# Optimization experiments

Hardware: AMD Instinct MI355X
Metric: run time of the kernel (lower is better)

The kernel has to match this reference:

```python
import jax, jax.numpy as jnp
import numpy as np

H = 2048      # hidden_size
NH = 16       # num attention heads
KVH = 4       # num kv heads (GQA)
D = 128       # head_dim
E = 32        # num experts
K = 4         # top-k experts per token
I = 768       # moe intermediate size
T = 1024      # num tokens (single prefill sequence)
EPS = 1e-6
THETA = 10000.0


def rmsnorm(x, w, eps=EPS):
    return x * jax.lax.rsqrt(jnp.mean(x * x, axis=-1, keepdims=True) + eps) * w


def rope_cos_sin(positions, dim, theta):
    inv_freq = 1.0 / (theta ** (jnp.arange(0, dim, 2, dtype=jnp.float32) / dim))
    freqs = positions.astype(jnp.float32)[:, None] * inv_freq[None, :]   # [T, D/2]
    emb = jnp.concatenate([freqs, freqs], axis=-1)                       # [T, D]
    return jnp.cos(emb), jnp.sin(emb)


def apply_rope(x, cos, sin):
    # x: [T, nH, D]; cos/sin: [T, D] -> neox style: cat(-x2, x1)
    x1, x2 = jnp.split(x, 2, axis=-1)
    x_rot = jnp.concatenate([-x2, x1], axis=-1)
    return cos[:, None, :] * x + sin[:, None, :] * x_rot


def setup_inputs() -> dict:
    key = jax.random.key(0)
    ks = jax.random.split(key, 8)
    s = 0.02
    return {
        "hidden_states": jax.random.normal(ks[0], (T, H), jnp.float32),
        "positions": jnp.arange(T, dtype=jnp.int32),
        "ln1_w": jnp.ones((H,), jnp.float32),
        "w_qkv": jax.random.normal(ks[1], ((NH + 2 * KVH) * D, H), jnp.float32) * s,
        "q_norm_w": jnp.ones((D,), jnp.float32),
        "k_norm_w": jnp.ones((D,), jnp.float32),
        "w_o": jax.random.normal(ks[2], (H, NH * D), jnp.float32) * s,
        "ln2_w": jnp.ones((H,), jnp.float32),
        "router_w": jax.random.normal(ks[3], (E, H), jnp.float32) * s,
        "w_gate": jax.random.normal(ks[4], (E, I, H), jnp.float32) * s,
        "w_up": jax.random.normal(ks[5], (E, I, H), jnp.float32) * s,
        "w_down": jax.random.normal(ks[6], (E, H, I), jnp.float32) * s,
    }


def decoder_layer(hidden_states, positions, ln1_w, w_qkv, q_norm_w, k_norm_w,
                  w_o, ln2_w, router_w, w_gate, w_up, w_down):
    # ---- attention block ----
    residual = hidden_states
    h = rmsnorm(hidden_states, ln1_w)

    qkv = h @ w_qkv.T                                      # [T, (NH+2*KVH)*D]
    q, k, v = jnp.split(qkv, [NH * D, (NH + KVH) * D], axis=-1)
    q = q.reshape(T, NH, D)
    k = k.reshape(T, KVH, D)
    v = v.reshape(T, KVH, D)

    # per-head RMSNorm on q and k (Qwen3 QK-norm)
    q = rmsnorm(q, q_norm_w)
    k = rmsnorm(k, k_norm_w)

    cos, sin = rope_cos_sin(positions, D, THETA)
    q = apply_rope(q, cos, sin)
    k = apply_rope(k, cos, sin)

    rep = NH // KVH
    k = jnp.repeat(k, rep, axis=1)                         # [T, NH, D]
    v = jnp.repeat(v, rep, axis=1)

    scale = D ** -0.5
    scores = jnp.einsum("qhd,khd->hqk", q, k) * scale      # [NH, T, T]
    causal = jnp.tril(jnp.ones((T, T), bool))
    scores = jnp.where(causal[None], scores, -1e30)
    probs = jax.nn.softmax(scores, axis=-1)
    attn = jnp.einsum("hqk,khd->qhd", probs, v).reshape(T, NH * D)
    attn_out = attn @ w_o.T                                # [T, H]

    hidden = residual + attn_out

    # ---- MoE block ----
    residual = hidden
    h = rmsnorm(hidden, ln2_w)

    logits = h @ router_w.T                                # [T, E]
    router_probs = jax.nn.softmax(logits, axis=-1)
    topk_w, topk_idx = jax.lax.top_k(router_probs, K)      # softmax-then-topk
    topk_w = topk_w / (jnp.sum(topk_w, axis=-1, keepdims=True) + 1e-20)

    # scatter top-k weights into a dense [T, E] combine matrix
    combine = jnp.zeros((T, E), h.dtype).at[
        jnp.arange(T)[:, None], topk_idx].add(topk_w)

    gate = jnp.einsum("th,eih->tei", h, w_gate)            # [T, E, I]
    up = jnp.einsum("th,eih->tei", h, w_up)
    act = jax.nn.silu(gate) * up
    moe_out = jnp.einsum("tei,ehi,te->th", act, w_down, combine)

    return residual + moe_out


def reference(hidden_states, positions, ln1_w, w_qkv, q_norm_w, k_norm_w,
              w_o, ln2_w, router_w, w_gate, w_up, w_down):
    return decoder_layer(hidden_states, positions, ln1_w, w_qkv, q_norm_w,
                         k_norm_w, w_o, ln2_w, router_w, w_gate, w_up, w_down)
```

## Files before the change

kernel.cpp:

```cpp
#include <hip/hip_runtime.h>

typedef __attribute__((ext_vector_type(4))) float f32x4;
typedef __attribute__((ext_vector_type(8))) __bf16 bf16x8;
typedef __attribute__((ext_vector_type(4))) __bf16 bf16x4;

__device__ __forceinline__ f32x4 mfma16(bf16x8 a, bf16x8 b, f32x4 c) {
  return __builtin_amdgcn_mfma_f32_16x16x32_bf16(a, b, c, 0, 0, 0);
}

__global__ __launch_bounds__(256) void rmsnorm_k(const float* __restrict__ x,
                                                 const float* __restrict__ w,
                                                 float* __restrict__ y,
                                                 __bf16* __restrict__ yb) {
  int t = blockIdx.x;
  const float* xr = x + (size_t)t * 2048;
  int d0 = threadIdx.x * 4;
  float4 v1 = *(const float4*)(xr + d0);
  float4 v2 = *(const float4*)(xr + 1024 + d0);
  float ss = v1.x*v1.x + v1.y*v1.y + v1.z*v1.z + v1.w*v1.w
           + v2.x*v2.x + v2.y*v2.y + v2.z*v2.z + v2.w*v2.w;
#pragma unroll
  for (int mk = 1; mk < 64; mk <<= 1) ss += __shfl_xor(ss, mk);
  __shared__ float red[4];
  if ((threadIdx.x & 63) == 0) red[threadIdx.x >> 6] = ss;
  __syncthreads();
  float tot = red[0] + red[1] + red[2] + red[3];
  float rs = rsqrtf(tot * (1.0f / 2048.0f) + 1e-6f);
  float* yr = y + (size_t)t * 2048;
  float4 w1 = *(const float4*)(w + d0);
  float4 w2 = *(const float4*)(w + 1024 + d0);
  float4 o1, o2;
  o1.x = v1.x*rs*w1.x; o1.y = v1.y*rs*w1.y; o1.z = v1.z*rs*w1.z; o1.w = v1.w*rs*w1.w;
  o2.x = v2.x*rs*w2.x; o2.y = v2.y*rs*w2.y; o2.z = v2.z*rs*w2.z; o2.w = v2.w*rs*w2.w;
  *(float4*)(yr + d0) = o1;
  *(float4*)(yr + 1024 + d0) = o2;
  if (yb) {
    bf16x4 b1, b2;
    b1[0] = (__bf16)o1.x; b1[1] = (__bf16)o1.y; b1[2] = (__bf16)o1.z; b1[3] = (__bf16)o1.w;
    b2[0] = (__bf16)o2.x; b2[1] = (__bf16)o2.y; b2[2] = (__bf16)o2.z; b2[3] = (__bf16)o2.w;
    *(bf16x4*)(yb + (size_t)t * 2048 + d0) = b1;
    *(bf16x4*)(yb + (size_t)t * 2048 + 1024 + d0) = b2;
  }
}

__global__ __launch_bounds__(256) void gemm3_k(const float* __restrict__ A,
                                               const float* __restrict__ B,
                                               const float* __restrict__ RESID,
                                               float* __restrict__ C, int N, int K) {
  __shared__ __align__(16) __bf16 sm[4 * 128 * 40];
  const int m0 = blockIdx.x * 128, n0 = blockIdx.y * 128;
  const int tid = threadIdx.x, l = tid & 63, w = tid >> 6;
  const int wm = w >> 1, wn = w & 1;
  __bf16* Ah = sm;         __bf16* Al = sm + 5120;
  __bf16* Bh = sm + 10240; __bf16* Bl = sm + 15360;
  f32x4 acc[4][4] = {};
  for (int kt = 0; kt < K; kt += 32) {
    __syncthreads();
#pragma unroll
    for (int i = 0; i < 4; i++) {
      int c = tid + i * 256;
      int row = c >> 3, k4 = c & 7;
      float4 v = *(const float4*)(A + (size_t)(m0 + row) * K + kt + k4 * 4);
      bf16x4 hv, lv;
#pragma unroll
      for (int j = 0; j < 4; j++) {
        float f = ((const float*)&v)[j];
        __bf16 h = (__bf16)f; hv[j] = h; lv[j] = (__bf16)(f - (float)h);
      }
      *(bf16x4*)(Ah + row * 40 + k4 * 4) = hv;
      *(bf16x4*)(Al + row * 40 + k4 * 4) = lv;
      float4 u = *(const float4*)(B + (size_t)(n0 + row) * K + kt + k4 * 4);
      bf16x4 hu, lu;
#pragma unroll
      for (int j = 0; j < 4; j++) {
        float f = ((const float*)&u)[j];
        __bf16 h = (__bf16)f; hu[j] = h; lu[j] = (__bf16)(f - (float)h);
      }
      *(bf16x4*)(Bh + row * 40 + k4 * 4) = hu;
      *(bf16x4*)(Bl + row * 40 + k4 * 4) = lu;
    }
    __syncthreads();
    bf16x8 ah[4], al[4], bh[4], bl[4];
    const int ko = (l >> 4) * 8;
#pragma unroll
    for (int f = 0; f < 4; f++) {
      int ar = wm * 64 + f * 16 + (l & 15);
      int br = wn * 64 + f * 16 + (l & 15);
      ah[f] = *(const bf16x8*)(Ah + ar * 40 + ko);
      al[f] = *(const bf16x8*)(Al + ar * 40 + ko);
      bh[f] = *(const bf16x8*)(Bh + br * 40 + ko);
      bl[f] = *(const bf16x8*)(Bl + br * 40 + ko);
    }
#pragma unroll
    for (int mf = 0; mf < 4; mf++)
#pragma unroll
      for (int nf = 0; nf < 4; nf++) {
        acc[mf][nf] = mfma16(ah[mf], bh[nf], acc[mf][nf]);
        acc[mf][nf] = mfma16(ah[mf], bl[nf], acc[mf][nf]);
        acc[mf][nf] = mfma16(al[mf], bh[nf], acc[mf][nf]);
      }
  }
#pragma unroll
  for (int mf = 0; mf < 4; mf++) {
    int row = m0 + wm * 64 + mf * 16 + ((l >> 4) << 2);
#pragma unroll
    for (int nf = 0; nf < 4; nf++) {
      int col = n0 + wn * 64 + nf * 16 + (l & 15);
#pragma unroll
      for (int r = 0; r < 4; r++) {
        float v = acc[mf][nf][r];
        if (RESID) v += RESID[(size_t)(row + r) * N + col];
        C[(size_t)(row + r) * N + col] = v;
      }
    }
  }
}

__global__ __launch_bounds__(128) void qkr_k(const float* __restrict__ qkv,
                                             const int* __restrict__ pos,
                                             const float* __restrict__ qw,
                                             const float* __restrict__ kw,
                                             __bf16* __restrict__ qh, __bf16* __restrict__ ql,
                                             __bf16* __restrict__ kh, __bf16* __restrict__ kl,
                                             __bf16* __restrict__ vh, __bf16* __restrict__ vl) {
  int hs = blockIdx.x, t = blockIdx.y, d = threadIdx.x;
  float x = qkv[(size_t)t * 3072 + hs * 128 + d];
  __shared__ float xs[128];
  __shared__ float red[2];
  float o;
  if (hs < 20) {
    float ss = x * x;
#pragma unroll
    for (int mk = 1; mk < 64; mk <<= 1) ss += __shfl_xor(ss, mk);
    if ((d & 63) == 0) red[d >> 6] = ss;
    __syncthreads();
    float rs = rsqrtf((red[0] + red[1]) * (1.0f / 128.0f) + 1e-6f);
    const float* w = (hs < 16) ? qw : kw;
    float xn = x * rs * w[d];
    xs[d] = xn;
    __syncthreads();
    int i = d & 63;
    float invf = (float)pow(10000.0, -(double)i / 64.0);
    float ang = (float)pos[t] * invf;
    float cf = (float)cos((double)ang);
    float sf = (float)sin((double)ang);
    float rot = (d < 64) ? -xs[d + 64] : xs[d - 64];
    o = cf * xn + sf * rot;
  } else {
    o = x;
  }
  __bf16 hi = (__bf16)o;
  __bf16 lo = (__bf16)(o - (float)hi);
  if (hs < 16) {
    size_t idx = ((size_t)hs * 1024 + t) * 128 + d;
    qh[idx] = hi; ql[idx] = lo;
  } else if (hs < 20) {
    size_t idx = ((size_t)(hs - 16) * 1024 + t) * 128 + d;
    kh[idx] = hi; kl[idx] = lo;
  } else {
    size_t idx = ((size_t)(hs - 20) * 1024 + t) * 128 + d;
    vh[idx] = hi; vl[idx] = lo;
  }
}

__global__ void vtrans_k(const __bf16* __restrict__ vh, const __bf16* __restrict__ vl,
                         __bf16* __restrict__ vhT, __bf16* __restrict__ vlT) {
  __shared__ __bf16 tile[32][33];
  int kv = blockIdx.z, t0 = blockIdx.x * 32, d0 = blockIdx.y * 32;
  int tx = threadIdx.x, ty = threadIdx.y;
  tile[ty][tx] = vh[((size_t)kv * 1024 + t0 + ty) * 128 + d0 + tx];
  __syncthreads();
  vhT[((size_t)kv * 128 + d0 + ty) * 1024 + t0 + tx] = tile[tx][ty];
  __syncthreads();
  tile[ty][tx] = vl[((size_t)kv * 1024 + t0 + ty) * 128 + d0 + tx];
  __syncthreads();
  vlT[((size_t)kv * 128 + d0 + ty) * 1024 + t0 + tx] = tile[tx][ty];
}

__global__ __launch_bounds__(256) void flash_k(const __bf16* __restrict__ qh, const __bf16* __restrict__ ql,
                                               const __bf16* __restrict__ kh, const __bf16* __restrict__ kl,
                                               const __bf16* __restrict__ vhT, const __bf16* __restrict__ vlT,
                                               float* __restrict__ attn) {
  constexpr int KH = 0, KL = 4352, VH = 8704, VL = 13824, PH = 18944, PL = 21504;
  __shared__ __align__(16) __bf16 sm[24064];
  const int qt = blockIdx.x, h = blockIdx.y;
  const int q0 = qt * 64, kvh = h >> 2;
  const int tid = threadIdx.x, l = tid & 63, w = tid >> 6;
  for (int c = tid; c < 1024; c += 256) {
    int row = c >> 4, dc = c & 15;
    size_t g = ((size_t)h * 1024 + q0 + row) * 128 + dc * 8;
// ... 130 lines not shown
    float mx = v;
#pragma unroll
    for (int mk = 1; mk < 32; mk <<= 1) mx = fmaxf(mx, __shfl_xor(mx, mk));
    float ex = (l < 32) ? expf(v - mx) : 0.0f;
    float den = ex;
#pragma unroll
    for (int mk = 1; mk < 32; mk <<= 1) den += __shfl_xor(den, mk);
    float prob = ex / den;
    float pv = v;
    int sel_i[4]; float sel_w[4]; float wsum = 0.0f;
#pragma unroll
    for (int j = 0; j < 4; j++) {
      float m2 = pv;
#pragma unroll
      for (int mk = 1; mk < 32; mk <<= 1) m2 = fmaxf(m2, __shfl_xor(m2, mk));
      unsigned long long ball = __ballot((pv == m2) && (l < 32));
      int sel = __ffsll(ball) - 1;
      float ps = __shfl(prob, sel);
      sel_i[j] = sel; sel_w[j] = ps; wsum += ps;
      if (l == sel) pv = -3e38f;
    }
    if (l < 4) {
      tidx[t * 4 + l] = sel_i[l];
      tw[t * 4 + l] = sel_w[l] / (wsum + 1e-20f);
      atomicAdd(&counts[sel_i[l]], 1);
    }
  }
}

__global__ void zero_k(int* counts) { if (threadIdx.x < 32) counts[threadIdx.x] = 0; }

__global__ void scan_k(const int* __restrict__ counts, int* __restrict__ offs,
                       int* __restrict__ cursor, int* __restrict__ pair_e,
                       int* __restrict__ pair_mt) {
  int l = threadIdx.x;
  int c = (l < 32) ? counts[l] : 0;
  int x = c;
#pragma unroll
  for (int d = 1; d < 32; d <<= 1) {
    int y = __shfl_up(x, d);
    if (l >= d) x += y;
  }
  if (l < 32) { offs[l] = x - c; cursor[l] = 0; }
  if (l == 31) offs[32] = x;
  if (l == 0) {
    int n = 0;
    for (int e = 0; e < 32; e++) {
      int ce = counts[e];
      for (int m = 0; m * 128 < ce; m++) { pair_e[n] = e; pair_mt[n] = m; n++; }
    }
    for (; n < 64; n++) { pair_e[n] = -1; pair_mt[n] = 0; }
  }
}

__global__ __launch_bounds__(256) void scatter_k(const int* __restrict__ tidx,
                                                 const int* __restrict__ offs,
                                                 int* __restrict__ cursor,
                                                 int* __restrict__ row_of_slot,
                                                 int* __restrict__ tok_of_row) {
  int p = blockIdx.x * 256 + threadIdx.x;
  if (p >= 4096) return;
  int e = tidx[p];
  int pos = atomicAdd(&cursor[e], 1);
  int row = offs[e] + pos;
  row_of_slot[p] = row;
  tok_of_row[row] = p >> 2;
}

__global__ __launch_bounds__(256) void gateup_k(const __bf16* __restrict__ h2b,
                                                const float* __restrict__ wg,
                                                const float* __restrict__ wu,
                                                const int* __restrict__ counts,
                                                const int* __restrict__ offs,
                                                const int* __restrict__ tok_of_row,
                                                const int* __restrict__ pair_e,
                                                const int* __restrict__ pair_mt,
                                                float* __restrict__ gu) {
  const int p = blockIdx.y;
  const int e = pair_e[p];
  if (e < 0) return;
  const int mt = pair_mt[p];
  const int cnt = counts[e];
  const int j = blockIdx.x;
  const float* wsel = (j < 6) ? wg : wu;
  const int n0 = (j < 6 ? j : j - 6) * 128;
  const int gout = (j < 6) ? 0 : 768;
  __shared__ __align__(16) __bf16 smA[128 * 40];
  __shared__ __align__(16) __bf16 smB[128 * 40];
  __shared__ int toks[128];
  const int tid = threadIdx.x, l = tid & 63, w = tid >> 6;
  const int wm = w >> 1, wn = w & 1;
  if (tid < 128) {
    int r = mt * 128 + tid;
    toks[tid] = (r < cnt) ? tok_of_row[offs[e] + r] : tok_of_row[offs[e]];
  }
  __syncthreads();
  const float* we = wsel + (size_t)e * 768 * 2048;
  bf16x8 ra[2]; float4 rb[4];
#pragma unroll
  for (int i = 0; i < 2; i++) {
    int c = tid + i * 256, row = c >> 2, kc = c & 3;
    ra[i] = *(const bf16x8*)(h2b + (size_t)toks[row] * 2048 + kc * 8);
  }
#pragma unroll
  for (int i = 0; i < 4; i++) {
    int c = tid + i * 256, row = c >> 3, k4 = c & 7;
    rb[i] = *(const float4*)(we + (size_t)(n0 + row) * 2048 + k4 * 4);
  }
  f32x4 acc[4][4] = {};
  for (int kt = 0; kt < 2048; kt += 32) {
    __syncthreads();
#pragma unroll
    for (int i = 0; i < 2; i++) {
      int c = tid + i * 256, row = c >> 2, kc = c & 3;
      *(bf16x8*)(smA + row * 40 + kc * 8) = ra[i];
    }
#pragma unroll
    for (int i = 0; i < 4; i++) {
      int c = tid + i * 256, row = c >> 3, k4 = c & 7;
      bf16x4 hv;
#pragma unroll
      for (int q = 0; q < 4; q++) hv[q] = (__bf16)((const float*)&rb[i])[q];
      *(bf16x4*)(smB + row * 40 + k4 * 4) = hv;
    }
    __syncthreads();
    if (kt + 32 < 2048) {
#pragma unroll
      for (int i = 0; i < 2; i++) {
        int c = tid + i * 256, row = c >> 2, kc = c & 3;
        ra[i] = *(const bf16x8*)(h2b + (size_t)toks[row] * 2048 + kt + 32 + kc * 8);
      }
#pragma unroll
      for (int i = 0; i < 4; i++) {
        int c = tid + i * 256, row = c >> 3, k4 = c & 7;
        rb[i] = *(const float4*)(we + (size_t)(n0 + row) * 2048 + kt + 32 + k4 * 4);
      }
    }
    bf16x8 af[4], bf_[4];
    const int ko = (l >> 4) * 8;
#pragma unroll
    for (int f = 0; f < 4; f++) {
      af[f]  = *(const bf16x8*)(smA + (wm * 64 + f * 16 + (l & 15)) * 40 + ko);
      bf_[f] = *(const bf16x8*)(smB + (wn * 64 + f * 16 + (l & 15)) * 40 + ko);
    }
#pragma unroll
    for (int mf = 0; mf < 4; mf++)
#pragma unroll
      for (int nf = 0; nf < 4; nf++)
        acc[mf][nf] = mfma16(af[mf], bf_[nf], acc[mf][nf]);
  }
#pragma unroll
  for (int mf = 0; mf < 4; mf++) {
    int rr = mt * 128 + wm * 64 + mf * 16 + ((l >> 4) << 2);
#pragma unroll
    for (int nf = 0; nf < 4; nf++) {
      int col = gout + n0 + wn * 64 + nf * 16 + (l & 15);
#pragma unroll
      for (int r = 0; r < 4; r++)
        if (rr + r < cnt)
          gu[(size_t)(offs[e] + rr + r) * 1536 + col] = acc[mf][nf][r];
    }
  }
}

__global__ __launch_bounds__(192) void silu_k(const float* __restrict__ gu,
                                              __bf16* __restrict__ act) {
  int r = blockIdx.x, c = threadIdx.x * 4;
  float4 g = *(const float4*)(gu + (size_t)r * 1536 + c);
  float4 u = *(const float4*)(gu + (size_t)r * 1536 + 768 + c);
  bf16x4 o;
  o[0] = (__bf16)(g.x / (1.0f + expf(-g.x)) * u.x);
  o[1] = (__bf16)(g.y / (1.0f + expf(-g.y)) * u.y);
  o[2] = (__bf16)(g.z / (1.0f + expf(-g.z)) * u.z);
  o[3] = (__bf16)(g.w / (1.0f + expf(-g.w)) * u.w);
  *(bf16x4*)(act + (size_t)r * 768 + c) = o;
}

__global__ __launch_bounds__(256) void down_k(const __bf16* __restrict__ act,
                                              const float* __restrict__ wd,
                                              const int* __restrict__ counts,
                                              const int* __restrict__ offs,
                                              const int* __restrict__ pair_e,
                                              const int* __restrict__ pair_mt,
                                              float* __restrict__ dout) {
  const int p = blockIdx.y;
  const int e = pair_e[p];
  if (e < 0) return;
  const int mt = pair_mt[p];
  const int cnt = counts[e];
  const int n0 = blockIdx.x * 128;
  __shared__ __align__(16) __bf16 smA[128 * 40];
  __shared__ __align__(16) __bf16 smB[128 * 40];
  const int tid = threadIdx.x, l = tid & 63, w = tid >> 6;
  const int wm = w >> 1, wn = w & 1;
  const float* wde = wd + (size_t)e * 2048 * 768;
  const int base = offs[e] + mt * 128;
  bf16x8 ra[2]; float4 rb[4];
#pragma unroll
  for (int i = 0; i < 2; i++) {
    int c = tid + i * 256, row = c >> 2, kc = c & 3;
    int rg = base + row; if (rg > 4095) rg = 4095;
    ra[i] = *(const bf16x8*)(act + (size_t)rg * 768 + kc * 8);
  }
#pragma unroll
  for (int i = 0; i < 4; i++) {
    int c = tid + i * 256, row = c >> 3, k4 = c & 7;
    rb[i] = *(const float4*)(wde + (size_t)(n0 + row) * 768 + k4 * 4);
  }
  f32x4 acc[4][4] = {};
  for (int kt = 0; kt < 768; kt += 32) {
    __syncthreads();
#pragma unroll
    for (int i = 0; i < 2; i++) {
      int c = tid + i * 256, row = c >> 2, kc = c & 3;
      *(bf16x8*)(smA + row * 40 + kc * 8) = ra[i];
    }
#pragma unroll
    for (int i = 0; i < 4; i++) {
      int c = tid + i * 256, row = c >> 3, k4 = c & 7;
      bf16x4 hv;
#pragma unroll
      for (int q = 0; q < 4; q++) hv[q] = (__bf16)((const float*)&rb[i])[q];
      *(bf16x4*)(smB + row * 40 + k4 * 4) = hv;
    }
    __syncthreads();
    if (kt + 32 < 768) {
#pragma unroll
      for (int i = 0; i < 2; i++) {
        int c = tid + i * 256, row = c >> 2, kc = c & 3;
        int rg = base + row; if (rg > 4095) rg = 4095;
        ra[i] = *(const bf16x8*)(act + (size_t)rg * 768 + kt + 32 + kc * 8);
      }
#pragma unroll
      for (int i = 0; i < 4; i++) {
        int c = tid + i * 256, row = c >> 3, k4 = c & 7;
        rb[i] = *(const float4*)(wde + (size_t)(n0 + row) * 768 + kt + 32 + k4 * 4);
      }
    }
    bf16x8 af[4], bf_[4];
    const int ko = (l >> 4) * 8;
#pragma unroll
    for (int f = 0; f < 4; f++) {
      af[f]  = *(const bf16x8*)(smA + (wm * 64 + f * 16 + (l & 15)) * 40 + ko);
      bf_[f] = *(const bf16x8*)(smB + (wn * 64 + f * 16 + (l & 15)) * 40 + ko);
    }
#pragma unroll
    for (int mf = 0; mf < 4; mf++)
#pragma unroll
      for (int nf = 0; nf < 4; nf++)
        acc[mf][nf] = mfma16(af[mf], bf_[nf], acc[mf][nf]);
  }
#pragma unroll
  for (int mf = 0; mf < 4; mf++) {
    int rr = mt * 128 + wm * 64 + mf * 16 + ((l >> 4) << 2);
#pragma unroll
    for (int nf = 0; nf < 4; nf++) {
      int col = n0 + wn * 64 + nf * 16 + (l & 15);
#pragma unroll
      for (int r = 0; r < 4; r++)
        if (rr + r < cnt)
          dout[(size_t)(offs[e] + rr + r) * 2048 + col] = acc[mf][nf][r];
    }
  }
}

__global__ __launch_bounds__(256) void combine_k(const float* __restrict__ hidden,
                                                 const float* __restrict__ dout,
                                                 const int* __restrict__ row_of_slot,
                                                 const float* __restrict__ tw,
                                                 float* __restrict__ out) {
  int t = blockIdx.x;
  int r0 = row_of_slot[t * 4 + 0], r1 = row_of_slot[t * 4 + 1];
  int r2 = row_of_slot[t * 4 + 2], r3 = row_of_slot[t * 4 + 3];
  float w0 = tw[t * 4 + 0], w1 = tw[t * 4 + 1], w2 = tw[t * 4 + 2], w3 = tw[t * 4 + 3];
  const float* h = hidden + (size_t)t * 2048;
  float* o = out + (size_t)t * 2048;
  for (int d = threadIdx.x * 4; d < 2048; d += 1024) {
    float4 hv = *(const float4*)(h + d);
    float4 a0 = *(const float4*)(dout + (size_t)r0 * 2048 + d);
    float4 a1 = *(const float4*)(dout + (size_t)r1 * 2048 + d);
    float4 a2 = *(const float4*)(dout + (size_t)r2 * 2048 + d);
    float4 a3 = *(const float4*)(dout + (size_t)r3 * 2048 + d);
    float4 ov;
    ov.x = hv.x + w0 * a0.x + w1 * a1.x + w2 * a2.x + w3 * a3.x;
    ov.y = hv.y + w0 * a0.y + w1 * a1.y + w2 * a2.y + w3 * a3.y;
    ov.z = hv.z + w0 * a0.z + w1 * a1.z + w2 * a2.z + w3 * a3.z;
    ov.w = hv.w + w0 * a0.w + w1 * a1.w + w2 * a2.w + w3 * a3.w;
    *(float4*)(o + d) = ov;
  }
}

extern "C" void kernel_launch(void* const* d_in, const int* in_sizes, int n_in,
                              void* d_out, int out_size, void* d_ws, size_t ws_size,
                              hipStream_t stream) {
  (void)in_sizes; (void)n_in; (void)out_size; (void)ws_size;
  const float* hs   = (const float*)d_in[0];
  const int*   pos  = (const int*)d_in[1];
  const float* ln1w = (const float*)d_in[2];
  const float* wqkv = (const float*)d_in[3];
  const float* qnw  = (const float*)d_in[4];
  const float* knw  = (const float*)d_in[5];
  const float* wo   = (const float*)d_in[6];
  const float* ln2w = (const float*)d_in[7];
  const float* rw   = (const float*)d_in[8];
  const float* wg   = (const float*)d_in[9];
  const float* wu   = (const float*)d_in[10];
  const float* wd   = (const float*)d_in[11];
  float* out = (float*)d_out;
  char* ws = (char*)d_ws;

  float*  h1     = (float*)(ws + 0);
  float*  gu     = (float*)(ws + 0);
  float*  dout   = (float*)(ws + 0);
  float*  qkv    = (float*)(ws + 8388608);
  __bf16* qh     = (__bf16*)(ws + 20971520);
  __bf16* ql     = (__bf16*)(ws + 25165824);
  __bf16* kh     = (__bf16*)(ws + 29360128);
  __bf16* kl     = (__bf16*)(ws + 30408704);
  __bf16* vh     = (__bf16*)(ws + 31457280);
  __bf16* vl     = (__bf16*)(ws + 32505856);
  __bf16* vhT    = (__bf16*)(ws + 33554432);
  __bf16* vlT    = (__bf16*)(ws + 34603008);
  int*    pair_e = (int*)(ws + 33554432);
  int*    pair_mt= (int*)(ws + 33554944);
  float*  attn   = (float*)(ws + 35651584);
  __bf16* h2b    = (__bf16*)(ws + 35651584);
  __bf16* act    = (__bf16*)(ws + 35651584);
  float*  hidden = (float*)(ws + 44040192);
  float*  h2     = (float*)(ws + 52428800);
  int*    tidx   = (int*)(ws + 60817408);
  float*  tw     = (float*)(ws + 60833792);
  int*    counts = (int*)(ws + 60850176);
  int*    offs   = (int*)(ws + 60850432);
  int*    cursor = (int*)(ws + 60850688);
  int*    row_of_slot = (int*)(ws + 60850944);
  int*    tok_of_row  = (int*)(ws + 60867328);

  rmsnorm_k<<<1024, 256, 0, stream>>>(hs, ln1w, h1, nullptr);
  gemm3_k<<<dim3(8, 24), 256, 0, stream>>>(h1, wqkv, nullptr, qkv, 3072, 2048);
  qkr_k<<<dim3(24, 1024), 128, 0, stream>>>(qkv, pos, qnw, knw, qh, ql, kh, kl, vh, vl);
  vtrans_k<<<dim3(32, 4, 4), dim3(32, 32), 0, stream>>>(vh, vl, vhT, vlT);
  flash_k<<<dim3(16, 16), 256, 0, stream>>>(qh, ql, kh, kl, vhT, vlT, attn);
  gemm3_k<<<dim3(8, 16), 256, 0, stream>>>(attn, wo, hs, hidden, 2048, 2048);

  rmsnorm_k<<<1024, 256, 0, stream>>>(hidden, ln2w, h2, h2b);
  zero_k<<<1, 64, 0, stream>>>(counts);
  router_k<<<1024, 256, 0, stream>>>(h2, rw, tidx, tw, counts);
  scan_k<<<1, 64, 0, stream>>>(counts, offs, cursor, pair_e, pair_mt);
  scatter_k<<<16, 256, 0, stream>>>(tidx, offs, cursor, row_of_slot, tok_of_row);
  gateup_k<<<dim3(12, 64), 256, 0, stream>>>(h2b, wg, wu, counts, offs, tok_of_row, pair_e, pair_mt, gu);
  silu_k<<<4096, 192, 0, stream>>>(gu, act);
  down_k<<<dim3(16, 64), 256, 0, stream>>>(act, wd, counts, offs, pair_e, pair_mt, dout);
  combine_k<<<1024, 256, 0, stream>>>(hidden, dout, row_of_slot, tw, out);
}
```

Measured before the change: 658.0 us.

## Halve GEMM N-tile to 64 and add register prefetch to dense GEMM

Shrinks the N tile of the dense split-bf16 GEMM and the MoE gate/up and down GEMMs from 128 to 64 columns, doubling grid size so more workgroups fill the CUs. The dense GEMM also gains a register double-buffer that loads the next K-slice from global memory while the current slice is being computed. Smaller tiles mean the A tile is reloaded twice as often, which adds global traffic and lowers arithmetic intensity per block.

```diff
diff --git a/kernel.cpp b/kernel.cpp
--- a/kernel.cpp
+++ b/kernel.cpp
@@ -47,54 +47,82 @@
                                                const float* __restrict__ B,
                                                const float* __restrict__ RESID,
                                                float* __restrict__ C, int N, int K) {
-  __shared__ __align__(16) __bf16 sm[4 * 128 * 40];
-  const int m0 = blockIdx.x * 128, n0 = blockIdx.y * 128;
+  __shared__ __align__(16) __bf16 smAh[128 * 40];
+  __shared__ __align__(16) __bf16 smAl[128 * 40];
+  __shared__ __align__(16) __bf16 smBh[64 * 40];
+  __shared__ __align__(16) __bf16 smBl[64 * 40];
+  const int m0 = blockIdx.x * 128, n0 = blockIdx.y * 64;
   const int tid = threadIdx.x, l = tid & 63, w = tid >> 6;
   const int wm = w >> 1, wn = w & 1;
-  __bf16* Ah = sm;         __bf16* Al = sm + 5120;
-  __bf16* Bh = sm + 10240; __bf16* Bl = sm + 15360;
-  f32x4 acc[4][4] = {};
+  float4 ra[4], rb[2];
+#pragma unroll
+  for (int i = 0; i < 4; i++) {
+    int c = tid + i * 256, row = c >> 3, k4 = c & 7;
+    ra[i] = *(const float4*)(A + (size_t)(m0 + row) * K + k4 * 4);
+  }
+#pragma unroll
+  for (int i = 0; i < 2; i++) {
+    int c = tid + i * 256, row = c >> 3, k4 = c & 7;
+    rb[i] = *(const float4*)(B + (size_t)(n0 + row) * K + k4 * 4);
+  }
+  f32x4 acc[4][2] = {};
   for (int kt = 0; kt < K; kt += 32) {
     __syncthreads();
 #pragma unroll
     for (int i = 0; i < 4; i++) {
-      int c = tid + i * 256;
-      int row = c >> 3, k4 = c & 7;
-      float4 v = *(const float4*)(A + (size_t)(m0 + row) * K + kt + k4 * 4);
+      int c = tid + i * 256, row = c >> 3, k4 = c & 7;
       bf16x4 hv, lv;
 #pragma unroll
       for (int j = 0; j < 4; j++) {
-        float f = ((const float*)&v)[j];
+        float f = ((const float*)&ra[i])[j];
         __bf16 h = (__bf16)f; hv[j] = h; lv[j] = (__bf16)(f - (float)h);
       }
-      *(bf16x4*)(Ah + row * 40 + k4 * 4) = hv;
-      *(bf16x4*)(Al + row * 40 + k4 * 4) = lv;
-      float4 u = *(const float4*)(B + (size_t)(n0 + row) * K + kt + k4 * 4);
-      bf16x4 hu, lu;
+      *(bf16x4*)(smAh + row * 40 + k4 * 4) = hv;
+      *(bf16x4*)(smAl + row * 40 + k4 * 4) = lv;
+    }
+#pragma unroll
+    for (int i = 0; i < 2; i++) {
+      int c = tid + i * 256, row = c >> 3, k4 = c & 7;
+      bf16x4 hv, lv;
 #pragma unroll
       for (int j = 0; j < 4; j++) {
-        float f = ((const float*)&u)[j];
-        __bf16 h = (__bf16)f; hu[j] = h; lu[j] = (__bf16)(f - (float)h);
-      }
-      *(bf16x4*)(Bh + row * 40 + k4 * 4) = hu;
-      *(bf16x4*)(Bl + row * 40 + k4 * 4) = lu;
-    }
-    __syncthreads();
-    bf16x8 ah[4], al[4], bh[4], bl[4];
+        float f = ((const float*)&rb[i])[j];
+        __bf16 h = (__bf16)f; hv[j] = h; lv[j] = (__bf16)(f - (float)h);
+      }
+      *(bf16x4*)(smBh + row * 40 + k4 * 4) = hv;
+      *(bf16x4*)(smBl + row * 40 + k4 * 4) = lv;
+    }
+    __syncthreads();
+    if (kt + 32 < K) {
+#pragma unroll
+      for (int i = 0; i < 4; i++) {
+        int c = tid + i * 256, row = c >> 3, k4 = c & 7;
+        ra[i] = *(const float4*)(A + (size_t)(m0 + row) * K + kt + 32 + k4 * 4);
+      }
+#pragma unroll
+      for (int i = 0; i < 2; i++) {
+        int c = tid + i * 256, row = c >> 3, k4 = c & 7;
+        rb[i] = *(const float4*)(B + (size_t)(n0 + row) * K + kt + 32 + k4 * 4);
+      }
+    }
+    bf16x8 ah[4], al[4], bh[2], bl[2];
     const int ko = (l >> 4) * 8;
 #pragma unroll
     for (int f = 0; f < 4; f++) {
       int ar = wm * 64 + f * 16 + (l & 15);
-      int br = wn * 64 + f * 16 + (l & 15);
-      ah[f] = *(const bf16x8*)(Ah + ar * 40 + ko);
-      al[f] = *(const bf16x8*)(Al + ar * 40 + ko);
-      bh[f] = *(const bf16x8*)(Bh + br * 40 + ko);
-      bl[f] = *(const bf16x8*)(Bl + br * 40 + ko);
+      ah[f] = *(const bf16x8*)(smAh + ar * 40 + ko);
+      al[f] = *(const bf16x8*)(smAl + ar * 40 + ko);
+    }
+#pragma unroll
+    for (int f = 0; f < 2; f++) {
+      int br = wn * 32 + f * 16 + (l & 15);
+      bh[f] = *(const bf16x8*)(smBh + br * 40 + ko);
+      bl[f] = *(const bf16x8*)(smBl + br * 40 + ko);
     }
 #pragma unroll
     for (int mf = 0; mf < 4; mf++)
 #pragma unroll
-      for (int nf = 0; nf < 4; nf++) {
+      for (int nf = 0; nf < 2; nf++) {
         acc[mf][nf] = mfma16(ah[mf], bh[nf], acc[mf][nf]);
         acc[mf][nf] = mfma16(ah[mf], bl[nf], acc[mf][nf]);
         acc[mf][nf] = mfma16(al[mf], bh[nf], acc[mf][nf]);
@@ -104,8 +132,8 @@
   for (int mf = 0; mf < 4; mf++) {
     int row = m0 + wm * 64 + mf * 16 + ((l >> 4) << 2);
 #pragma unroll
-    for (int nf = 0; nf < 4; nf++) {
-      int col = n0 + wn * 64 + nf * 16 + (l & 15);
+    for (int nf = 0; nf < 2; nf++) {
+      int col = n0 + wn * 32 + nf * 16 + (l & 15);
 #pragma unroll
       for (int r = 0; r < 4; r++) {
         float v = acc[mf][nf][r];
@@ -402,11 +430,11 @@
   const int mt = pair_mt[p];
   const int cnt = counts[e];
   const int j = blockIdx.x;
-  const float* wsel = (j < 6) ? wg : wu;
-  const int n0 = (j < 6 ? j : j - 6) * 128;
-  const int gout = (j < 6) ? 0 : 768;
+  const float* wsel = (j < 12) ? wg : wu;
+  const int n0 = (j < 12 ? j : j - 12) * 64;
+  const int gout = (j < 12) ? 0 : 768;
   __shared__ __align__(16) __bf16 smA[128 * 40];
-  __shared__ __align__(16) __bf16 smB[128 * 40];
+  __shared__ __align__(16) __bf16 smB[64 * 40];
   __shared__ int toks[128];
   const int tid = threadIdx.x, l = tid & 63, w = tid >> 6;
   const int wm = w >> 1, wn = w & 1;
@@ -416,18 +444,18 @@
   }
   __syncthreads();
   const float* we = wsel + (size_t)e * 768 * 2048;
-  bf16x8 ra[2]; float4 rb[4];
+  bf16x8 ra[2]; float4 rb[2];
 #pragma unroll
   for (int i = 0; i < 2; i++) {
     int c = tid + i * 256, row = c >> 2, kc = c & 3;
     ra[i] = *(const bf16x8*)(h2b + (size_t)toks[row] * 2048 + kc * 8);
   }
 #pragma unroll
-  for (int i = 0; i < 4; i++) {
+  for (int i = 0; i < 2; i++) {
     int c = tid + i * 256, row = c >> 3, k4 = c & 7;
     rb[i] = *(const float4*)(we + (size_t)(n0 + row) * 2048 + k4 * 4);
   }
-  f32x4 acc[4][4] = {};
+  f32x4 acc[4][2] = {};
   for (int kt = 0; kt < 2048; kt += 32) {
     __syncthreads();
 #pragma unroll
@@ -436,7 +464,7 @@
       *(bf16x8*)(smA + row * 40 + kc * 8) = ra[i];
     }
 #pragma unroll
-    for (int i = 0; i < 4; i++) {
+    for (int i = 0; i < 2; i++) {
       int c = tid + i * 256, row = c >> 3, k4 = c & 7;
       bf16x4 hv;
 #pragma unroll
@@ -451,30 +479,31 @@
         ra[i] = *(const bf16x8*)(h2b + (size_t)toks[row] * 2048 + kt + 32 + kc * 8);
       }
 #pragma unroll
-      for (int i = 0; i < 4; i++) {
+      for (int i = 0; i < 2; i++) {
         int c = tid + i * 256, row = c >> 3, k4 = c & 7;
         rb[i] = *(const float4*)(we + (size_t)(n0 + row) * 2048 + kt + 32 + k4 * 4);
       }
     }
-    bf16x8 af[4], bf_[4];
+    bf16x8 af[4], bf_[2];
     const int ko = (l >> 4) * 8;
 #pragma unroll
-    for (int f = 0; f < 4; f++) {
-      af[f]  = *(const bf16x8*)(smA + (wm * 64 + f * 16 + (l & 15)) * 40 + ko);
-      bf_[f] = *(const bf16x8*)(smB + (wn * 64 + f * 16 + (l & 15)) * 40 + ko);
-    }
+    for (int f = 0; f < 4; f++)
+      af[f] = *(const bf16x8*)(smA + (wm * 64 + f * 16 + (l & 15)) * 40 + ko);
+#pragma unroll
+    for (int f = 0; f < 2; f++)
+      bf_[f] = *(const bf16x8*)(smB + (wn * 32 + f * 16 + (l & 15)) * 40 + ko);
 #pragma unroll
     for (int mf = 0; mf < 4; mf++)
 #pragma unroll
-      for (int nf = 0; nf < 4; nf++)
+      for (int nf = 0; nf < 2; nf++)
         acc[mf][nf] = mfma16(af[mf], bf_[nf], acc[mf][nf]);
   }
 #pragma unroll
   for (int mf = 0; mf < 4; mf++) {
     int rr = mt * 128 + wm * 64 + mf * 16 + ((l >> 4) << 2);
 #pragma unroll
-    for (int nf = 0; nf < 4; nf++) {
-      int col = gout + n0 + wn * 64 + nf * 16 + (l & 15);
+    for (int nf = 0; nf < 2; nf++) {
+      int col = gout + n0 + wn * 32 + nf * 16 + (l & 15);
 #pragma unroll
       for (int r = 0; r < 4; r++)
         if (rr + r < cnt)
@@ -508,14 +537,14 @@
   if (e < 0) return;
   const int mt = pair_mt[p];
   const int cnt = counts[e];
-  const int n0 = blockIdx.x * 128;
+  const int n0 = blockIdx.x * 64;
   __shared__ __align__(16) __bf16 smA[128 * 40];
-  __shared__ __align__(16) __bf16 smB[128 * 40];
+  __shared__ __align__(16) __bf16 smB[64 * 40];
   const int tid = threadIdx.x, l = tid & 63, w = tid >> 6;
   const int wm = w >> 1, wn = w & 1;
   const float* wde = wd + (size_t)e * 2048 * 768;
   const int base = offs[e] + mt * 128;
-  bf16x8 ra[2]; float4 rb[4];
+  bf16x8 ra[2]; float4 rb[2];
 #pragma unroll
   for (int i = 0; i < 2; i++) {
     int c = tid + i * 256, row = c >> 2, kc = c & 3;
@@ -523,11 +552,11 @@
     ra[i] = *(const bf16x8*)(act + (size_t)rg * 768 + kc * 8);
   }
 #pragma unroll
-  for (int i = 0; i < 4; i++) {
+  for (int i = 0; i < 2; i++) {
     int c = tid + i * 256, row = c >> 3, k4 = c & 7;
     rb[i] = *(const float4*)(wde + (size_t)(n0 + row) * 768 + k4 * 4);
   }
-  f32x4 acc[4][4] = {};
+  f32x4 acc[4][2] = {};
   for (int kt = 0; kt < 768; kt += 32) {
     __syncthreads();
 #pragma unroll
@@ -536,7 +565,7 @@
       *(bf16x8*)(smA + row * 40 + kc * 8) = ra[i];
     }
 #pragma unroll
-    for (int i = 0; i < 4; i++) {
+    for (int i = 0; i < 2; i++) {
       int c = tid + i * 256, row = c >> 3, k4 = c & 7;
       bf16x4 hv;
 #pragma unroll
@@ -552,30 +581,31 @@
         ra[i] = *(const bf16x8*)(act + (size_t)rg * 768 + kt + 32 + kc * 8);
       }
 #pragma unroll
-      for (int i = 0; i < 4; i++) {
+      for (int i = 0; i < 2; i++) {
         int c = tid + i * 256, row = c >> 3, k4 = c & 7;
         rb[i] = *(const float4*)(wde + (size_t)(n0 + row) * 768 + kt + 32 + k4 * 4);
       }
     }
-    bf16x8 af[4], bf_[4];
+    bf16x8 af[4], bf_[2];
     const int ko = (l >> 4) * 8;
 #pragma unroll
-    for (int f = 0; f < 4; f++) {
-      af[f]  = *(const bf16x8*)(smA + (wm * 64 + f * 16 + (l & 15)) * 40 + ko);
-      bf_[f] = *(const bf16x8*)(smB + (wn * 64 + f * 16 + (l & 15)) * 40 + ko);
-    }
+    for (int f = 0; f < 4; f++)
+      af[f] = *(const bf16x8*)(smA + (wm * 64 + f * 16 + (l & 15)) * 40 + ko);
+#pragma unroll
+    for (int f = 0; f < 2; f++)
+      bf_[f] = *(const bf16x8*)(smB + (wn * 32 + f * 16 + (l & 15)) * 40 + ko);
 #pragma unroll
     for (int mf = 0; mf < 4; mf++)
 #pragma unroll
-      for (int nf = 0; nf < 4; nf++)
+      for (int nf = 0; nf < 2; nf++)
         acc[mf][nf] = mfma16(af[mf], bf_[nf], acc[mf][nf]);
   }
 #pragma unroll
   for (int mf = 0; mf < 4; mf++) {
     int rr = mt * 128 + wm * 64 + mf * 16 + ((l >> 4) << 2);
 #pragma unroll
-    for (int nf = 0; nf < 4; nf++) {
-      int col = n0 + wn * 64 + nf * 16 + (l & 15);
+    for (int nf = 0; nf < 2; nf++) {
+      int col = n0 + wn * 32 + nf * 16 + (l & 15);
 #pragma unroll
       for (int r = 0; r < 4; r++)
         if (rr + r < cnt)
@@ -657,19 +687,19 @@
   int*    tok_of_row  = (int*)(ws + 60867328);
 
   rmsnorm_k<<<1024, 256, 0, stream>>>(hs, ln1w, h1, nullptr);
-  gemm3_k<<<dim3(8, 24), 256, 0, stream>>>(h1, wqkv, nullptr, qkv, 3072, 2048);
+  gemm3_k<<<dim3(8, 48), 256, 0, stream>>>(h1, wqkv, nullptr, qkv, 3072, 2048);
   qkr_k<<<dim3(24, 1024), 128, 0, stream>>>(qkv, pos, qnw, knw, qh, ql, kh, kl, vh, vl);
   vtrans_k<<<dim3(32, 4, 4), dim3(32, 32), 0, stream>>>(vh, vl, vhT, vlT);
   flash_k<<<dim3(16, 16), 256, 0, stream>>>(qh, ql, kh, kl, vhT, vlT, attn);
-  gemm3_k<<<dim3(8, 16), 256, 0, stream>>>(attn, wo, hs, hidden, 2048, 2048);
+  gemm3_k<<<dim3(8, 32), 256, 0, stream>>>(attn, wo, hs, hidden, 2048, 2048);
 
   rmsnorm_k<<<1024, 256, 0, stream>>>(hidden, ln2w, h2, h2b);
   zero_k<<<1, 64, 0, stream>>>(counts);
   router_k<<<1024, 256, 0, stream>>>(h2, rw, tidx, tw, counts);
   scan_k<<<1, 64, 0, stream>>>(counts, offs, cursor, pair_e, pair_mt);
   scatter_k<<<16, 256, 0, stream>>>(tidx, offs, cursor, row_of_slot, tok_of_row);
-  gateup_k<<<dim3(12, 64), 256, 0, stream>>>(h2b, wg, wu, counts, offs, tok_of_row, pair_e, pair_mt, gu);
+  gateup_k<<<dim3(24, 64), 256, 0, stream>>>(h2b, wg, wu, counts, offs, tok_of_row, pair_e, pair_mt, gu);
   silu_k<<<4096, 192, 0, stream>>>(gu, act);
-  down_k<<<dim3(16, 64), 256, 0, stream>>>(act, wd, counts, offs, pair_e, pair_mt, dout);
+  down_k<<<dim3(32, 64), 256, 0, stream>>>(act, wd, counts, offs, pair_e, pair_mt, dout);
   combine_k<<<1024, 256, 0, stream>>>(hidden, dout, row_of_slot, tw, out);
 }
```

Result: faster. 610.0 us (-7.3%).

## Double-buffer MoE GEMM LDS tiles and prefetch in split-bf16 dense GEMM

Applied to the files above, without the earlier changes.

The dense split-bf16 GEMM now uses 128x64 tiles, which doubles the grid for the QKV and output projections, and it prefetches the next K-slice of global data into registers while the current one is computed. The MoE gate/up and down kernels switch to double-buffered shared memory with loads issued two steps ahead and one barrier per iteration, so global loads and LDS writes overlap the MFMA work. This costs more LDS and registers per block, which may lower occupancy, and the smaller dense tiles reuse each loaded tile less.

```diff
diff --git a/kernel.cpp b/kernel.cpp
--- a/kernel.cpp
+++ b/kernel.cpp
@@ -47,54 +47,82 @@
                                                const float* __restrict__ B,
                                                const float* __restrict__ RESID,
                                                float* __restrict__ C, int N, int K) {
-  __shared__ __align__(16) __bf16 sm[4 * 128 * 40];
-  const int m0 = blockIdx.x * 128, n0 = blockIdx.y * 128;
+  __shared__ __align__(16) __bf16 smAh[128 * 40];
+  __shared__ __align__(16) __bf16 smAl[128 * 40];
+  __shared__ __align__(16) __bf16 smBh[64 * 40];
+  __shared__ __align__(16) __bf16 smBl[64 * 40];
+  const int m0 = blockIdx.x * 128, n0 = blockIdx.y * 64;
   const int tid = threadIdx.x, l = tid & 63, w = tid >> 6;
   const int wm = w >> 1, wn = w & 1;
-  __bf16* Ah = sm;         __bf16* Al = sm + 5120;
-  __bf16* Bh = sm + 10240; __bf16* Bl = sm + 15360;
-  f32x4 acc[4][4] = {};
+  float4 ra[4], rb[2];
+#pragma unroll
+  for (int i = 0; i < 4; i++) {
+    int c = tid + i * 256, row = c >> 3, k4 = c & 7;
+    ra[i] = *(const float4*)(A + (size_t)(m0 + row) * K + k4 * 4);
+  }
+#pragma unroll
+  for (int i = 0; i < 2; i++) {
+    int c = tid + i * 256, row = c >> 3, k4 = c & 7;
+    rb[i] = *(const float4*)(B + (size_t)(n0 + row) * K + k4 * 4);
+  }
+  f32x4 acc[4][2] = {};
   for (int kt = 0; kt < K; kt += 32) {
     __syncthreads();
 #pragma unroll
     for (int i = 0; i < 4; i++) {
-      int c = tid + i * 256;
-      int row = c >> 3, k4 = c & 7;
-      float4 v = *(const float4*)(A + (size_t)(m0 + row) * K + kt + k4 * 4);
+      int c = tid + i * 256, row = c >> 3, k4 = c & 7;
       bf16x4 hv, lv;
 #pragma unroll
       for (int j = 0; j < 4; j++) {
-        float f = ((const float*)&v)[j];
+        float f = ((const float*)&ra[i])[j];
         __bf16 h = (__bf16)f; hv[j] = h; lv[j] = (__bf16)(f - (float)h);
       }
-      *(bf16x4*)(Ah + row * 40 + k4 * 4) = hv;
-      *(bf16x4*)(Al + row * 40 + k4 * 4) = lv;
-      float4 u = *(const float4*)(B + (size_t)(n0 + row) * K + kt + k4 * 4);
-      bf16x4 hu, lu;
+      *(bf16x4*)(smAh + row * 40 + k4 * 4) = hv;
+      *(bf16x4*)(smAl + row * 40 + k4 * 4) = lv;
+    }
+#pragma unroll
+    for (int i = 0; i < 2; i++) {
+      int c = tid + i * 256, row = c >> 3, k4 = c & 7;
+      bf16x4 hv, lv;
 #pragma unroll
       for (int j = 0; j < 4; j++) {
-        float f = ((const float*)&u)[j];
-        __bf16 h = (__bf16)f; hu[j] = h; lu[j] = (__bf16)(f - (float)h);
-      }
-      *(bf16x4*)(Bh + row * 40 + k4 * 4) = hu;
-      *(bf16x4*)(Bl + row * 40 + k4 * 4) = lu;
-    }
-    __syncthreads();
-    bf16x8 ah[4], al[4], bh[4], bl[4];
+        float f = ((const float*)&rb[i])[j];
+        __bf16 h = (__bf16)f; hv[j] = h; lv[j] = (__bf16)(f - (float)h);
+      }
+      *(bf16x4*)(smBh + row * 40 + k4 * 4) = hv;
+      *(bf16x4*)(smBl + row * 40 + k4 * 4) = lv;
+    }
+    __syncthreads();
+    if (kt + 32 < K) {
+#pragma unroll
+      for (int i = 0; i < 4; i++) {
+        int c = tid + i * 256, row = c >> 3, k4 = c & 7;
+        ra[i] = *(const float4*)(A + (size_t)(m0 + row) * K + kt + 32 + k4 * 4);
+      }
+#pragma unroll
+      for (int i = 0; i < 2; i++) {
+        int c = tid + i * 256, row = c >> 3, k4 = c & 7;
+        rb[i] = *(const float4*)(B + (size_t)(n0 + row) * K + kt + 32 + k4 * 4);
+      }
+    }
+    bf16x8 ah[4], al[4], bh[2], bl[2];
     const int ko = (l >> 4) * 8;
 #pragma unroll
     for (int f = 0; f < 4; f++) {
       int ar = wm * 64 + f * 16 + (l & 15);
-      int br = wn * 64 + f * 16 + (l & 15);
-      ah[f] = *(const bf16x8*)(Ah + ar * 40 + ko);
-      al[f] = *(const bf16x8*)(Al + ar * 40 + ko);
-      bh[f] = *(const bf16x8*)(Bh + br * 40 + ko);
-      bl[f] = *(const bf16x8*)(Bl + br * 40 + ko);
+      ah[f] = *(const bf16x8*)(smAh + ar * 40 + ko);
+      al[f] = *(const bf16x8*)(smAl + ar * 40 + ko);
+    }
+#pragma unroll
+    for (int f = 0; f < 2; f++) {
+      int br = wn * 32 + f * 16 + (l & 15);
+      bh[f] = *(const bf16x8*)(smBh + br * 40 + ko);
+      bl[f] = *(const bf16x8*)(smBl + br * 40 + ko);
     }
 #pragma unroll
     for (int mf = 0; mf < 4; mf++)
 #pragma unroll
-      for (int nf = 0; nf < 4; nf++) {
+      for (int nf = 0; nf < 2; nf++) {
         acc[mf][nf] = mfma16(ah[mf], bh[nf], acc[mf][nf]);
         acc[mf][nf] = mfma16(ah[mf], bl[nf], acc[mf][nf]);
         acc[mf][nf] = mfma16(al[mf], bh[nf], acc[mf][nf]);
@@ -104,8 +132,8 @@
   for (int mf = 0; mf < 4; mf++) {
     int row = m0 + wm * 64 + mf * 16 + ((l >> 4) << 2);
 #pragma unroll
-    for (int nf = 0; nf < 4; nf++) {
-      int col = n0 + wn * 64 + nf * 16 + (l & 15);
+    for (int nf = 0; nf < 2; nf++) {
+      int col = n0 + wn * 32 + nf * 16 + (l & 15);
 #pragma unroll
       for (int r = 0; r < 4; r++) {
         float v = acc[mf][nf][r];
@@ -405,8 +433,8 @@
   const float* wsel = (j < 6) ? wg : wu;
   const int n0 = (j < 6 ? j : j - 6) * 128;
   const int gout = (j < 6) ? 0 : 768;
-  __shared__ __align__(16) __bf16 smA[128 * 40];
-  __shared__ __align__(16) __bf16 smB[128 * 40];
+  __shared__ __align__(16) __bf16 smA[2][128 * 40];
+  __shared__ __align__(16) __bf16 smB[2][128 * 40];
   __shared__ int toks[128];
   const int tid = threadIdx.x, l = tid & 63, w = tid >> 6;
   const int wm = w >> 1, wn = w & 1;
@@ -416,59 +444,55 @@
   }
   __syncthreads();
   const float* we = wsel + (size_t)e * 768 * 2048;
-  bf16x8 ra[2]; float4 rb[4];
-#pragma unroll
-  for (int i = 0; i < 2; i++) {
-    int c = tid + i * 256, row = c >> 2, kc = c & 3;
-    ra[i] = *(const bf16x8*)(h2b + (size_t)toks[row] * 2048 + kc * 8);
-  }
-#pragma unroll
-  for (int i = 0; i < 4; i++) {
-    int c = tid + i * 256, row = c >> 3, k4 = c & 7;
-    rb[i] = *(const float4*)(we + (size_t)(n0 + row) * 2048 + k4 * 4);
-  }
+  bf16x8 ra[2][2];
+  float4 rb[2][4];
+
+#define GU_ISSUE(set, kt) do { \
+  _Pragma("unroll") \
+  for (int i = 0; i < 2; i++) { int c = tid + i * 256; \
+    ra[set][i] = *(const bf16x8*)(h2b + (size_t)toks[c >> 2] * 2048 + (kt) + (c & 3) * 8); } \
+  _Pragma("unroll") \
+  for (int i = 0; i < 4; i++) { int c = tid + i * 256; \
+    rb[set][i] = *(const float4*)(we + (size_t)(n0 + (c >> 3)) * 2048 + (kt) + (c & 7) * 4); } \
+} while (0)
+
+#define GU_WRITE(buf, set) do { \
+  _Pragma("unroll") \
+  for (int i = 0; i < 2; i++) { int c = tid + i * 256; \
+    *(bf16x8*)(&smA[buf][0] + (c >> 2) * 40 + (c & 3) * 8) = ra[set][i]; } \
+  _Pragma("unroll") \
+  for (int i = 0; i < 4; i++) { int c = tid + i * 256; bf16x4 hv; \
+    _Pragma("unroll") \
+    for (int q = 0; q < 4; q++) hv[q] = (__bf16)((const float*)&rb[set][i])[q]; \
+    *(bf16x4*)(&smB[buf][0] + (c >> 3) * 40 + (c & 7) * 4) = hv; } \
+} while (0)
+
+  GU_ISSUE(0, 0);
+  GU_ISSUE(1, 32);
+  GU_WRITE(0, 0);
+  __syncthreads();
+
   f32x4 acc[4][4] = {};
-  for (int kt = 0; kt < 2048; kt += 32) {
-    __syncthreads();
-#pragma unroll
-    for (int i = 0; i < 2; i++) {
-      int c = tid + i * 256, row = c >> 2, kc = c & 3;
-      *(bf16x8*)(smA + row * 40 + kc * 8) = ra[i];
-    }
-#pragma unroll
-    for (int i = 0; i < 4; i++) {
-      int c = tid + i * 256, row = c >> 3, k4 = c & 7;
-      bf16x4 hv;
-#pragma unroll
-      for (int q = 0; q < 4; q++) hv[q] = (__bf16)((const float*)&rb[i])[q];
-      *(bf16x4*)(smB + row * 40 + k4 * 4) = hv;
-    }
-    __syncthreads();
-    if (kt + 32 < 2048) {
-#pragma unroll
-      for (int i = 0; i < 2; i++) {
-        int c = tid + i * 256, row = c >> 2, kc = c & 3;
-        ra[i] = *(const bf16x8*)(h2b + (size_t)toks[row] * 2048 + kt + 32 + kc * 8);
-      }
-#pragma unroll
-      for (int i = 0; i < 4; i++) {
-        int c = tid + i * 256, row = c >> 3, k4 = c & 7;
-        rb[i] = *(const float4*)(we + (size_t)(n0 + row) * 2048 + kt + 32 + k4 * 4);
-      }
-    }
+  const int ko = (l >> 4) * 8;
+  for (int it = 0; it < 64; it++) {
+    const int buf = it & 1;
+    if (it + 1 < 64) GU_WRITE(buf ^ 1, (it + 1) & 1);
+    if (it + 2 < 64) GU_ISSUE(buf, (it + 2) * 32);
     bf16x8 af[4], bf_[4];
-    const int ko = (l >> 4) * 8;
 #pragma unroll
     for (int f = 0; f < 4; f++) {
-      af[f]  = *(const bf16x8*)(smA + (wm * 64 + f * 16 + (l & 15)) * 40 + ko);
-      bf_[f] = *(const bf16x8*)(smB + (wn * 64 + f * 16 + (l & 15)) * 40 + ko);
+      af[f]  = *(const bf16x8*)(&smA[buf][0] + (wm * 64 + f * 16 + (l & 15)) * 40 + ko);
+      bf_[f] = *(const bf16x8*)(&smB[buf][0] + (wn * 64 + f * 16 + (l & 15)) * 40 + ko);
     }
 #pragma unroll
     for (int mf = 0; mf < 4; mf++)
 #pragma unroll
       for (int nf = 0; nf < 4; nf++)
         acc[mf][nf] = mfma16(af[mf], bf_[nf], acc[mf][nf]);
-  }
+    __syncthreads();
+  }
+#undef GU_ISSUE
+#undef GU_WRITE
 #pragma unroll
   for (int mf = 0; mf < 4; mf++) {
     int rr = mt * 128 + wm * 64 + mf * 16 + ((l >> 4) << 2);
@@ -509,67 +533,62 @@
   const int mt = pair_mt[p];
   const int cnt = counts[e];
   const int n0 = blockIdx.x * 128;
-  __shared__ __align__(16) __bf16 smA[128 * 40];
-  __shared__ __align__(16) __bf16 smB[128 * 40];
+  __shared__ __align__(16) __bf16 smA[2][128 * 40];
+  __shared__ __align__(16) __bf16 smB[2][128 * 40];
   const int tid = threadIdx.x, l = tid & 63, w = tid >> 6;
   const int wm = w >> 1, wn = w & 1;
   const float* wde = wd + (size_t)e * 2048 * 768;
   const int base = offs[e] + mt * 128;
-  bf16x8 ra[2]; float4 rb[4];
-#pragma unroll
-  for (int i = 0; i < 2; i++) {
-    int c = tid + i * 256, row = c >> 2, kc = c & 3;
-    int rg = base + row; if (rg > 4095) rg = 4095;
-    ra[i] = *(const bf16x8*)(act + (size_t)rg * 768 + kc * 8);
-  }
-#pragma unroll
-  for (int i = 0; i < 4; i++) {
-    int c = tid + i * 256, row = c >> 3, k4 = c & 7;
-    rb[i] = *(const float4*)(wde + (size_t)(n0 + row) * 768 + k4 * 4);
-  }
+  bf16x8 ra[2][2];
+  float4 rb[2][4];
+
+#define DN_ISSUE(set, kt) do { \
+  _Pragma("unroll") \
+  for (int i = 0; i < 2; i++) { int c = tid + i * 256; \
+    int rg = base + (c >> 2); if (rg > 4095) rg = 4095; \
+    ra[set][i] = *(const bf16x8*)(act + (size_t)rg * 768 + (kt) + (c & 3) * 8); } \
+  _Pragma("unroll") \
+  for (int i = 0; i < 4; i++) { int c = tid + i * 256; \
+    rb[set][i] = *(const float4*)(wde + (size_t)(n0 + (c >> 3)) * 768 + (kt) + (c & 7) * 4); } \
+} while (0)
+
+#define DN_WRITE(buf, set) do { \
+  _Pragma("unroll") \
+  for (int i = 0; i < 2; i++) { int c = tid + i * 256; \
+    *(bf16x8*)(&smA[buf][0] + (c >> 2) * 40 + (c & 3) * 8) = ra[set][i]; } \
+  _Pragma("unroll") \
+  for (int i = 0; i < 4; i++) { int c = tid + i * 256; bf16x4 hv; \
+    _Pragma("unroll") \
+    for (int q = 0; q < 4; q++) hv[q] = (__bf16)((const float*)&rb[set][i])[q]; \
+    *(bf16x4*)(&smB[buf][0] + (c >> 3) * 40 + (c & 7) * 4) = hv; } \
+} while (0)
+
+  DN_ISSUE(0, 0);
+  DN_ISSUE(1, 32);
+  DN_WRITE(0, 0);
+  __syncthreads();
+
   f32x4 acc[4][4] = {};
-  for (int kt = 0; kt < 768; kt += 32) {
-    __syncthreads();
-#pragma unroll
-    for (int i = 0; i < 2; i++) {
-      int c = tid + i * 256, row = c >> 2, kc = c & 3;
-      *(bf16x8*)(smA + row * 40 + kc * 8) = ra[i];
-    }
-#pragma unroll
-    for (int i = 0; i < 4; i++) {
-      int c = tid + i * 256, row = c >> 3, k4 = c & 7;
-      bf16x4 hv;
-#pragma unroll
-      for (int q = 0; q < 4; q++) hv[q] = (__bf16)((const float*)&rb[i])[q];
-      *(bf16x4*)(smB + row * 40 + k4 * 4) = hv;
-    }
-    __syncthreads();
-    if (kt + 32 < 768) {
-#pragma unroll
-      for (int i = 0; i < 2; i++) {
-        int c = tid + i * 256, row = c >> 2, kc = c & 3;
-        int rg = base + row; if (rg > 4095) rg = 4095;
-        ra[i] = *(const bf16x8*)(act + (size_t)rg * 768 + kt + 32 + kc * 8);
-      }
-#pragma unroll
-      for (int i = 0; i < 4; i++) {
-        int c = tid + i * 256, row = c >> 3, k4 = c & 7;
-        rb[i] = *(const float4*)(wde + (size_t)(n0 + row) * 768 + kt + 32 + k4 * 4);
-      }
-    }
+  const int ko = (l >> 4) * 8;
+  for (int it = 0; it < 24; it++) {
+    const int buf = it & 1;
+    if (it + 1 < 24) DN_WRITE(buf ^ 1, (it + 1) & 1);
+    if (it + 2 < 24) DN_ISSUE(buf, (it + 2) * 32);
     bf16x8 af[4], bf_[4];
-    const int ko = (l >> 4) * 8;
 #pragma unroll
     for (int f = 0; f < 4; f++) {
-      af[f]  = *(const bf16x8*)(smA + (wm * 64 + f * 16 + (l & 15)) * 40 + ko);
-      bf_[f] = *(const bf16x8*)(smB + (wn * 64 + f * 16 + (l & 15)) * 40 + ko);
+      af[f]  = *(const bf16x8*)(&smA[buf][0] + (wm * 64 + f * 16 + (l & 15)) * 40 + ko);
+      bf_[f] = *(const bf16x8*)(&smB[buf][0] + (wn * 64 + f * 16 + (l & 15)) * 40 + ko);
     }
 #pragma unroll
     for (int mf = 0; mf < 4; mf++)
 #pragma unroll
       for (int nf = 0; nf < 4; nf++)
         acc[mf][nf] = mfma16(af[mf], bf_[nf], acc[mf][nf]);
-  }
+    __syncthreads();
+  }
+#undef DN_ISSUE
+#undef DN_WRITE
 #pragma unroll
   for (int mf = 0; mf < 4; mf++) {
     int rr = mt * 128 + wm * 64 + mf * 16 + ((l >> 4) << 2);
@@ -657,11 +676,11 @@
   int*    tok_of_row  = (int*)(ws + 60867328);
 
   rmsnorm_k<<<1024, 256, 0, stream>>>(hs, ln1w, h1, nullptr);
-  gemm3_k<<<dim3(8, 24), 256, 0, stream>>>(h1, wqkv, nullptr, qkv, 3072, 2048);
+  gemm3_k<<<dim3(8, 48), 256, 0, stream>>>(h1, wqkv, nullptr, qkv, 3072, 2048);
   qkr_k<<<dim3(24, 1024), 128, 0, stream>>>(qkv, pos, qnw, knw, qh, ql, kh, kl, vh, vl);
   vtrans_k<<<dim3(32, 4, 4), dim3(32, 32), 0, stream>>>(vh, vl, vhT, vlT);
   flash_k<<<dim3(16, 16), 256, 0, stream>>>(qh, ql, kh, kl, vhT, vlT, attn);
-  gemm3_k<<<dim3(8, 16), 256, 0, stream>>>(attn, wo, hs, hidden, 2048, 2048);
+  gemm3_k<<<dim3(8, 32), 256, 0, stream>>>(attn, wo, hs, hidden, 2048, 2048);
 
   rmsnorm_k<<<1024, 256, 0, stream>>>(hidden, ln2w, h2, h2b);
   zero_k<<<1, 64, 0, stream>>>(counts);
```

New measurement: 2.440 ms. 3.71x slower.
